# Optimization experiments

Measured on AMD Instinct MI355X. Metric: run time of the kernel, lower is better.

The kernel has to match this reference:

```python
import jax, jax.numpy as jnp
import numpy as np

B, D, H, E, K = 16384, 4096, 2048, 64, 2
TEMPERATURE = 0.8  # training=True


def setup_inputs() -> dict:
    key = jax.random.key(0)
    k1, k2, k3 = jax.random.split(key, 3)
    x = jax.random.normal(k1, (B, D), dtype=jnp.float32)
    W1 = jax.random.normal(k2, (H, D), dtype=jnp.float32) * 0.02
    b1 = jnp.zeros((H,), dtype=jnp.float32)
    W2 = jax.random.normal(k3, (E, H), dtype=jnp.float32) * 0.02
    b2 = jnp.zeros((E,), dtype=jnp.float32)
    return {"x": x, "W1": W1, "b1": b1, "W2": W2, "b2": b2}


def reference(x, W1, b1, W2, b2):
    # router MLP: Linear(D->H) -> ReLU -> Linear(H->E)
    h = jax.nn.relu(jnp.einsum('bd,hd->bh', x, W1) + b1)
    router_logits = jnp.einsum('bh,eh->be', h, W2) + b2  # [B, E]

    # temperature-scaled softmax for routing
    routing_probs = jax.nn.softmax(router_logits / TEMPERATURE, axis=1)
    routing_weights, expert_indices = jax.lax.top_k(routing_probs, K)  # [B, K]
    routing_weights = routing_weights / routing_weights.sum(axis=1, keepdims=True)

    # entropy-based uncertainty uses UN-scaled logits
    full_probs = jax.nn.softmax(router_logits, axis=1)
    entropy = -jnp.sum(full_probs * jnp.log(full_probs + 1e-10), axis=1).mean()
    uncertainty = entropy / jnp.log(jnp.float32(E))
    return routing_weights, expert_indices, uncertainty
```

## Files before the change

kernel.cpp:

```cpp
#include <hip/hip_runtime.h>
#include <hip/hip_bf16.h>
#include <math.h>

#define B_ROWS 16384
#define D_DIM  4096
#define H_DIM  2048
#define E_DIM  64
#define TEMP   0.8f

typedef __bf16 bf16x8 __attribute__((ext_vector_type(8)));
typedef float  f32x4  __attribute__((ext_vector_type(4)));
typedef unsigned short ushort8 __attribute__((ext_vector_type(8)));

__device__ __forceinline__ unsigned short bf_rne(float f) {
  unsigned u = __float_as_uint(f);
  u += 0x7FFF + ((u >> 16) & 1);
  return (unsigned short)(u >> 16);
}

__device__ __forceinline__ void async_copy16(const void* g, void* l) {
  __builtin_amdgcn_global_load_lds(
      (const __attribute__((address_space(1))) void*)g,
      (__attribute__((address_space(3))) void*)l, 16, 0, 0);
}

__global__ __launch_bounds__(256) void split_kernel(
    const float* __restrict__ in, unsigned short* __restrict__ hi,
    unsigned short* __restrict__ lo) {
  const size_t i = ((size_t)blockIdx.x * 256 + threadIdx.x) * 8;
  float4 v0 = *(const float4*)(in + i);
  float4 v1 = *(const float4*)(in + i + 4);
  float f[8] = {v0.x, v0.y, v0.z, v0.w, v1.x, v1.y, v1.z, v1.w};
  ushort8 hv, lv;
#pragma unroll
  for (int j = 0; j < 8; ++j) {
    unsigned short h = bf_rne(f[j]);
    float fh = __uint_as_float(((unsigned)h) << 16);
    hv[j] = h;
    lv[j] = bf_rne(f[j] - fh);
  }
  *(ushort8*)(hi + i) = hv;
  *(ushort8*)(lo + i) = lv;
}

#define G_BM 256
#define G_BN 256
#define G_BK 32
#define G_NT (D_DIM / G_BK)

#define MFMA_TRIPLE(MIv, NIv, FAH, FAL, FBH, FBL)                               \
  _Pragma("unroll")                                                             \
  for (int mf = 0; mf < 4; ++mf) {                                              \
    _Pragma("unroll")                                                           \
    for (int nf = 0; nf < 2; ++nf) {                                            \
      f32x4 a = acc[MIv][mf][NIv][nf];                                          \
      a = __builtin_amdgcn_mfma_f32_16x16x32_bf16(FAH[mf], FBH[nf], a, 0, 0, 0);\
      a = __builtin_amdgcn_mfma_f32_16x16x32_bf16(FAL[mf], FBH[nf], a, 0, 0, 0);\
      a = __builtin_amdgcn_mfma_f32_16x16x32_bf16(FAH[mf], FBL[nf], a, 0, 0, 0);\
      acc[MIv][mf][NIv][nf] = a;                                                \
    }                                                                           \
  }

__global__ __launch_bounds__(512, 2) void gemm1_8ph_kernel(
    const unsigned short* __restrict__ xh, const unsigned short* __restrict__ xl,
    const unsigned short* __restrict__ w1h, const unsigned short* __restrict__ w1l,
    const float* __restrict__ b1,
    unsigned short* __restrict__ hhp, unsigned short* __restrict__ hlp) {
  __shared__ unsigned short LAh[2 * 8192];
  __shared__ unsigned short LAl[2 * 8192];
  __shared__ unsigned short LBh[2 * 8192];
  __shared__ unsigned short LBl[2 * 8192];

  const int t    = threadIdx.x;
  const int lane = t & 63;
  const int w    = t >> 6;
  const int wm   = w >> 2;
  const int wn   = w & 3;

  const int wg   = blockIdx.x;
  const int xcd  = wg & 7;
  const int slot = wg >> 3;
  const int mt   = xcd * 8 + (slot >> 3);
  const int nt   = slot & 7;
  const int m0   = mt * G_BM;
  const int n0   = nt * G_BN;

  const int sr  = t >> 2;
  const int sc  = (t & 3) * 8;
  const int scs = sc ^ (((sr >> 1) & 3) << 3);
  const int t8  = t * 8;
  const unsigned short* gAh = xh  + (size_t)(m0 + sr) * D_DIM + scs;
  const unsigned short* gAl = xl  + (size_t)(m0 + sr) * D_DIM + scs;
  const unsigned short* gBh = w1h + (size_t)(n0 + sr) * D_DIM + scs;
  const unsigned short* gBl = w1l + (size_t)(n0 + sr) * D_DIM + scs;

  auto stageA = [&](int buf, int half, int kt) {
    const size_t go = (size_t)half * 128 * D_DIM + (size_t)kt * G_BK;
    const int lo = buf * 8192 + half * 4096 + t8;
    async_copy16(gAh + go, &LAh[lo]);
    async_copy16(gAl + go, &LAl[lo]);
  };
  auto stageB = [&](int buf, int half, int kt) {
    const size_t go = (size_t)half * 128 * D_DIM + (size_t)kt * G_BK;
    const int lo = buf * 8192 + half * 4096 + t8;
    async_copy16(gBh + go, &LBh[lo]);
    async_copy16(gBl + go, &LBl[lo]);
  };

  constexpr int SST[8] = {0,1,0,1,0,1,0,1};
  constexpr int SHF[8] = {1,1,0,0,1,1,0,0};
  constexpr int SBF[8] = {1,1,0,0,0,0,1,1};
  constexpr int STL[8] = {1,1,2,2,2,2,3,3};

  auto stagePhase = [&](int p, int i) {
    int tl = 2 * i + STL[p];
    if (tl > G_NT - 1) tl = G_NT - 1;
    if (SST[p] == 0) stageA(SBF[p], SHF[p], tl);
    else             stageB(SBF[p], SHF[p], tl);
  };

  const int fr = lane & 15;
  const int ko = (lane >> 4) * 8;
  const int fc = ko ^ (((fr >> 1) & 3) << 3);
  const int aO = (wm * 64 + fr) * 32 + fc;
  const int bO = (wn * 32 + fr) * 32 + fc;

  f32x4 acc[2][4][2][2];
#pragma unroll
  for (int a = 0; a < 2; ++a)
#pragma unroll
    for (int b = 0; b < 4; ++b)
#pragma unroll
      for (int c = 0; c < 2; ++c)
#pragma unroll
        for (int d = 0; d < 2; ++d) acc[a][b][c][d] = (f32x4)0.f;

  stageA(0, 0, 0); stageB(0, 0, 0);
  stageA(0, 1, 0); stageB(0, 1, 0);
  stageA(1, 0, 1); stageB(1, 0, 1);
  asm volatile("s_waitcnt vmcnt(4)" ::: "memory");
  __builtin_amdgcn_s_barrier();
  __builtin_amdgcn_sched_barrier(0);

  for (int i = 0; i < G_NT / 2; ++i) {
#pragma unroll
    for (int half = 0; half < 2; ++half) {
      const int base = half * 4;
      const int cb   = half * 8192;

      bf16x8 fah[4], fal[4];
      bf16x8 fbh0[2], fbl0[2];
      bf16x8 fbh1[2], fbl1[2];

#pragma unroll
      for (int mf = 0; mf < 4; ++mf) {
        fah[mf] = *(const bf16x8*)&LAh[cb + aO + mf * 512];
        fal[mf] = *(const bf16x8*)&LAl[cb + aO + mf * 512];
      }
#pragma unroll
      for (int nf = 0; nf < 2; ++nf) {
        fbh0[nf] = *(const bf16x8*)&LBh[cb + bO + nf * 512];
        fbl0[nf] = *(const bf16x8*)&LBl[cb + bO + nf * 512];
      }
      stagePhase(base + 0, i);
      __builtin_amdgcn_s_barrier();
      __builtin_amdgcn_sched_barrier(0);
      __builtin_amdgcn_s_setprio(1);
      MFMA_TRIPLE(0, 0, fah, fal, fbh0, fbl0)
      __builtin_amdgcn_s_setprio(0);
      __builtin_amdgcn_s_barrier();
      __builtin_amdgcn_sched_barrier(0);

#pragma unroll
      for (int nf = 0; nf < 2; ++nf) {
        fbh1[nf] = *(const bf16x8*)&LBh[cb + 4096 + bO + nf * 512];
        fbl1[nf] = *(const bf16x8*)&LBl[cb + 4096 + bO + nf * 512];
      }
      stagePhase(base + 1, i);
      __builtin_amdgcn_s_barrier();
      __builtin_amdgcn_sched_barrier(0);
      __builtin_amdgcn_s_setprio(1);
      MFMA_TRIPLE(0, 1, fah, fal, fbh1, fbl1)
      __builtin_amdgcn_s_setprio(0);
      __builtin_amdgcn_s_barrier();
      __builtin_amdgcn_sched_barrier(0);

#pragma unroll
      for (int mf = 0; mf < 4; ++mf) {
        fah[mf] = *(const bf16x8*)&LAh[cb + 4096 + aO + mf * 512];
        fal[mf] = *(const bf16x8*)&LAl[cb + 4096 + aO + mf * 512];
      }
      stagePhase(base + 2, i);
      __builtin_amdgcn_s_barrier();
      __builtin_amdgcn_sched_barrier(0);
      __builtin_amdgcn_s_setprio(1);
      MFMA_TRIPLE(1, 0, fah, fal, fbh0, fbl0)
      __builtin_amdgcn_s_setprio(0);
      __builtin_amdgcn_s_barrier();
      __builtin_amdgcn_sched_barrier(0);

      stagePhase(base + 3, i);
      __builtin_amdgcn_s_barrier();
      __builtin_amdgcn_sched_barrier(0);
      __builtin_amdgcn_s_setprio(1);
      MFMA_TRIPLE(1, 1, fah, fal, fbh1, fbl1)
      __builtin_amdgcn_s_setprio(0);
      asm volatile("s_waitcnt vmcnt(4)" ::: "memory");
      __builtin_amdgcn_s_barrier();
      __builtin_amdgcn_sched_barrier(0);
    }
  }
  asm volatile("s_waitcnt vmcnt(0)" ::: "memory");

#pragma unroll
  for (int mi = 0; mi < 2; ++mi)
#pragma unroll
    for (int ni = 0; ni < 2; ++ni)
#pragma unroll
      for (int nf = 0; nf < 2; ++nf) {
        const int nn = n0 + wn * 32 + ni * 128 + nf * 16 + fr;
        const float bias = b1[nn];
#pragma unroll
        for (int mf = 0; mf < 4; ++mf) {
          const int mb = m0 + wm * 64 + mi * 128 + mf * 16 + (lane >> 4) * 4;
#pragma unroll
          for (int r = 0; r < 4; ++r) {
            const float vv = fmaxf(acc[mi][mf][ni][nf][r] + bias, 0.f);
            const unsigned short hv = bf_rne(vv);
            const float fh = __uint_as_float(((unsigned)hv) << 16);
            const unsigned short lv = bf_rne(vv - fh);
            hhp[(size_t)(mb + r) * H_DIM + nn] = hv;
            hlp[(size_t)(mb + r) * H_DIM + nn] = lv;
          }
        }
      }
}

#define BM 128
#define BN 128
#define BKK 32

__global__ __launch_bounds__(256) void gemm1_fb_kernel(
    const float* __restrict__ x,
    const unsigned short* __restrict__ w1h,
    const unsigned short* __restrict__ w1l,
    const float* __restrict__ b1,
    unsigned short* __restrict__ hhp, unsigned short* __restrict__ hlp) {
  __shared__ unsigned short Ah[BM * BKK];
  __shared__ unsigned short Al[BM * BKK];
  __shared__ unsigned short Bh[BN * BKK];
  __shared__ unsigned short Bl[BN * BKK];

  const int t    = threadIdx.x;
  const int lane = t & 63;
  const int w    = t >> 6;
  const int wm   = w >> 1;
  const int wn   = w & 1;
  const int m0   = blockIdx.y * BM;
  const int n0   = blockIdx.x * BN;

  const int e0 = (w * 2 + 0) * 512 + lane * 8;
  const int e1 = (w * 2 + 1) * 512 + lane * 8;
  const int r0 = e0 >> 5, c0 = e0 & 31;
  const int r1 = e1 >> 5, c1 = e1 & 31;
  const unsigned short* bh_g0 = w1h + (size_t)(n0 + r0) * D_DIM + c0;
  const unsigned short* bh_g1 = w1h + (size_t)(n0 + r1) * D_DIM + c1;
  const unsigned short* bl_g0 = w1l + (size_t)(n0 + r0) * D_DIM + c0;
  const unsigned short* bl_g1 = w1l + (size_t)(n0 + r1) * D_DIM + c1;
  unsigned short* bh_l0 = &Bh[e0];
  unsigned short* bh_l1 = &Bh[e1];
  unsigned short* bl_l0 = &Bl[e0];
  unsigned short* bl_l1 = &Bl[e1];

  const int ar = t >> 1;
  const int ac = (t & 1) * 16;
  const float* xp = x + (size_t)(m0 + ar) * D_DIM + ac;
  unsigned short* ah_w = &Ah[ar * BKK + ac];
  unsigned short* al_w = &Al[ar * BKK + ac];

  const int koff = (lane >> 4) * 8;
  const unsigned short* a_rd[4];
  const unsigned short* b_rd[4];
#pragma unroll
  for (int f = 0; f < 4; ++f) {
    a_rd[f] = &Ah[(wm * 64 + f * 16 + (lane & 15)) * BKK + koff];
    b_rd[f] = &Bh[(wn * 64 + f * 16 + (lane & 15)) * BKK + koff];
  }
  const int lo_off_a = (int)(Al - Ah);
  const int lo_off_b = (int)(Bl - Bh);

  f32x4 acc[4][4];
#pragma unroll
  for (int i = 0; i < 4; ++i)
#pragma unroll
    for (int j = 0; j < 4; ++j) acc[i][j] = (f32x4)0.f;

  for (int k0 = 0; k0 < D_DIM; k0 += BKK) {
    async_copy16(bh_g0 + k0, bh_l0);
    async_copy16(bh_g1 + k0, bh_l1);
    async_copy16(bl_g0 + k0, bl_l0);
    async_copy16(bl_g1 + k0, bl_l1);

    float4 v[4];
#pragma unroll
    for (int j = 0; j < 4; ++j) v[j] = *(const float4*)(xp + k0 + j * 4);
    float f[16] = {v[0].x, v[0].y, v[0].z, v[0].w, v[1].x, v[1].y, v[1].z, v[1].w,
                   v[2].x, v[2].y, v[2].z, v[2].w, v[3].x, v[3].y, v[3].z, v[3].w};
    ushort8 hv0, hv1, lv0, lv1;
#pragma unroll
    for (int j = 0; j < 8; ++j) {
      unsigned short h = bf_rne(f[j]);
      float fh = __uint_as_float(((unsigned)h) << 16);
      hv0[j] = h;
      lv0[j] = bf_rne(f[j] - fh);
    }
#pragma unroll
    for (int j = 0; j < 8; ++j) {
      unsigned short h = bf_rne(f[8 + j]);
      float fh = __uint_as_float(((unsigned)h) << 16);
      hv1[j] = h;
      lv1[j] = bf_rne(f[8 + j] - fh);
    }
    *(ushort8*)(ah_w)     = hv0;
    *(ushort8*)(ah_w + 8) = hv1;
    *(ushort8*)(al_w)     = lv0;
    *(ushort8*)(al_w + 8) = lv1;

    __syncthreads();

    bf16x8 fa_h[4], fa_l[4], fb_h[4], fb_l[4];
#pragma unroll
    for (int ff = 0; ff < 4; ++ff) {
      fa_h[ff] = *(const bf16x8*)(a_rd[ff]);
      fa_l[ff] = *(const bf16x8*)(a_rd[ff] + lo_off_a);
      fb_h[ff] = *(const bf16x8*)(b_rd[ff]);
      fb_l[ff] = *(const bf16x8*)(b_rd[ff] + lo_off_b);
    }
#pragma unroll
    for (int i = 0; i < 4; ++i)
#pragma unroll
      for (int j = 0; j < 4; ++j) {
        acc[i][j] = __builtin_amdgcn_mfma_f32_16x16x32_bf16(fa_h[i], fb_h[j], acc[i][j], 0, 0, 0);
        acc[i][j] = __builtin_amdgcn_mfma_f32_16x16x32_bf16(fa_l[i], fb_h[j], acc[i][j], 0, 0, 0);
        acc[i][j] = __builtin_amdgcn_mfma_f32_16x16x32_bf16(fa_h[i], fb_l[j], acc[i][j], 0, 0, 0);
      }
    __syncthreads();
  }

#pragma unroll
  for (int fn = 0; fn < 4; ++fn) {
    const int n = n0 + wn * 64 + fn * 16 + (lane & 15);
    const float bias = b1[n];
#pragma unroll
    for (int fm = 0; fm < 4; ++fm) {
      const int mbase = m0 + wm * 64 + fm * 16 + (lane >> 4) * 4;
#pragma unroll
      for (int r = 0; r < 4; ++r) {
        const float vv = fmaxf(acc[fm][fn][r] + bias, 0.f);
        const unsigned short hv = bf_rne(vv);
        const float fh = __uint_as_float(((unsigned)hv) << 16);
        const unsigned short lv = bf_rne(vv - fh);
        hhp[(size_t)(mbase + r) * H_DIM + n] = hv;
        hlp[(size_t)(mbase + r) * H_DIM + n] = lv;
      }
    }
  }
}

#define F_BM 64
#define F_BK 64
#define F_NT (H_DIM / F_BK)

__global__ __launch_bounds__(256) void gemm2_router_kernel(
    const unsigned short* __restrict__ hhp,
    const unsigned short* __restrict__ hlp,
    const unsigned short* __restrict__ w2h,
    const unsigned short* __restrict__ w2l,
    const float* __restrict__ b2,
    float* __restrict__ out, float* __restrict__ accum) {
  __shared__ unsigned short Ahs[2 * 4096];
  __shared__ unsigned short Als[2 * 4096];
  __shared__ unsigned short Bhs[2 * 4096];
  __shared__ unsigned short Bls[2 * 4096];
  __shared__ float LG[F_BM][E_DIM + 1];

  const int t    = threadIdx.x;
  const int lane = t & 63;
  const int w    = t >> 6;
  const int m0   = blockIdx.x * F_BM;

  const int srow = w * 8 + (lane >> 3);
  const int scol = ((lane & 7) * 8) ^ (((lane >> 3) & 7) << 3);
  const int t8   = t * 8;
  const unsigned short* gAh = hhp + (size_t)(m0 + srow) * H_DIM + scol;
  const unsigned short* gAl = hlp + (size_t)(m0 + srow) * H_DIM + scol;
  const unsigned short* gBh = w2h + (size_t)srow * H_DIM + scol;
  const unsigned short* gBl = w2l + (size_t)srow * H_DIM + scol;

  auto stage2 = [&](int buf, int kt) {
    const size_t k0 = (size_t)kt * F_BK;
#pragma unroll
    for (int c = 0; c < 2; ++c) {
      const size_t go = k0 + (size_t)c * 32 * H_DIM;
      const int lo = buf * 4096 + c * 2048 + t8;
      async_copy16(gAh + go, &Ahs[lo]);
      async_copy16(gAl + go, &Als[lo]);
      async_copy16(gBh + go, &Bhs[lo]);
      async_copy16(gBl + go, &Bls[lo]);
    }
  };

  const int fr = lane & 15;
  const int ko = (lane >> 4) * 8;
  const int Ra = w * 16 + fr;
  int aoff[2], boff[2][4];
#pragma unroll
  for (int kk = 0; kk < 2; ++kk) {
    aoff[kk] = Ra * 64 + ((kk * 32 + ko) ^ ((Ra & 7) << 3));
#pragma unroll
    for (int f = 0; f < 4; ++f) {
      const int Rb = f * 16 + fr;
      boff[kk][f] = Rb * 64 + ((kk * 32 + ko) ^ ((Rb & 7) << 3));
    }
  }

  f32x4 acc[4];
#pragma unroll
  for (int f = 0; f < 4; ++f) acc[f] = (f32x4)0.f;

  stage2(0, 0);
  int buf = 0;
  for (int kt = 0; kt < F_NT; ++kt) {
    if (kt + 1 < F_NT) {
      stage2(buf ^ 1, kt + 1);
      asm volatile("s_waitcnt vmcnt(8)" ::: "memory");
    } else {
      asm volatile("s_waitcnt vmcnt(0)" ::: "memory");
    }
    __builtin_amdgcn_s_barrier();
    __builtin_amdgcn_sched_barrier(0);
    const int bo = buf * 4096;
#pragma unroll
    for (int kk = 0; kk < 2; ++kk) {
      bf16x8 fa_h = *(const bf16x8*)&Ahs[bo + aoff[kk]];
      bf16x8 fa_l = *(const bf16x8*)&Als[bo + aoff[kk]];
#pragma unroll
      for (int f = 0; f < 4; ++f) {
        bf16x8 fb_h = *(const bf16x8*)&Bhs[bo + boff[kk][f]];
        bf16x8 fb_l = *(const bf16x8*)&Bls[bo + boff[kk][f]];
        acc[f] = __builtin_amdgcn_mfma_f32_16x16x32_bf16(fa_h, fb_h, acc[f], 0, 0, 0);
        acc[f] = __builtin_amdgcn_mfma_f32_16x16x32_bf16(fa_l, fb_h, acc[f], 0, 0, 0);
        acc[f] = __builtin_amdgcn_mfma_f32_16x16x32_bf16(fa_h, fb_l, acc[f], 0, 0, 0);
      }
    }
    __builtin_amdgcn_s_barrier();
    __builtin_amdgcn_sched_barrier(0);
    buf ^= 1;
  }

#pragma unroll
  for (int f = 0; f < 4; ++f) {
    const int e = f * 16 + fr;
    const float bias = b2[e];
#pragma unroll
    for (int r = 0; r < 4; ++r) {
      const int ml = w * 16 + (lane >> 4) * 4 + r;
      LG[ml][e] = acc[f][r] + bias;
    }
  }
  __syncthreads();

  if (t < F_BM) {
    const int row = m0 + t;
    float l0 = LG[t][0]; int i0 = 0;
    float l1 = -INFINITY; int i1 = -1;
#pragma unroll
    for (int e = 1; e < E_DIM; ++e) {
      float v = LG[t][e];
      if (v > l0)      { l1 = l0; i1 = i0; l0 = v; i0 = e; }
      else if (v > l1) { l1 = v; i1 = e; }
    }

    const float eT = expf((l1 - l0) / TEMP);
    const float w0 = 1.f / (1.f + eT);
    const float w1 = eT / (1.f + eT);

    float Z = 0.f;
#pragma unroll
    for (int e = 0; e < E_DIM; ++e) Z += expf(LG[t][e] - l0);
    const float invZ = 1.f / Z;
    float ent = 0.f;
#pragma unroll
    for (int e = 0; e < E_DIM; ++e) {
      float p = expf(LG[t][e] - l0) * invZ;
      ent -= p * logf(p + 1e-10f);
    }

    out[(size_t)row * 2 + 0] = w0;
    out[(size_t)row * 2 + 1] = w1;
    out[(size_t)B_ROWS * 2 + (size_t)row * 2 + 0] = (float)i0;
    out[(size_t)B_ROWS * 2 + (size_t)row * 2 + 1] = (float)i1;

#pragma unroll
    for (int off = 32; off > 0; off >>= 1) ent += __shfl_down(ent, off);
    if (t == 0) atomicAdd(accum, ent);
  }
}

__global__ void zero_kernel(float* p) { p[0] = 0.f; }

__global__ void finalize_kernel(const float* __restrict__ accum,
                                float* __restrict__ out) {
  out[(size_t)B_ROWS * 4] = accum[0] / ((float)B_ROWS * logf((float)E_DIM));
}

extern "C" void kernel_launch(void* const* d_in, const int* in_sizes, int n_in,
                              void* d_out, int out_size, void* d_ws,
                              size_t ws_size, hipStream_t stream) {
  const float* x  = (const float*)d_in[0];
  const float* W1 = (const float*)d_in[1];
  const float* b1 = (const float*)d_in[2];
  const float* W2 = (const float*)d_in[3];
  const float* b2 = (const float*)d_in[4];
  float* out = (float*)d_out;

  const size_t SZ_W1 = (size_t)H_DIM * D_DIM;
  const size_t SZ_W2 = (size_t)E_DIM * H_DIM;
  const size_t SZ_H  = (size_t)B_ROWS * H_DIM;
  const size_t SZ_X  = (size_t)B_ROWS * D_DIM;

  unsigned short* w1h = (unsigned short*)d_ws;
  unsigned short* w1l = w1h + SZ_W1;
  unsigned short* w2h = w1l + SZ_W1;
  unsigned short* w2l = w2h + SZ_W2;
  unsigned short* hhp = w2l + SZ_W2;
  unsigned short* hlp = hhp + SZ_H;
  float* accum        = (float*)(hlp + SZ_H);
  unsigned short* xh  = (unsigned short*)(accum + 64);
  unsigned short* xl  = xh + SZ_X;
  const size_t need_bytes = (size_t)((char*)(xl + SZ_X) - (char*)d_ws);
  const bool fast = ws_size >= need_bytes;

  zero_kernel<<<1, 1, 0, stream>>>(accum);

  split_kernel<<<(int)(SZ_W1 / (256 * 8)), 256, 0, stream>>>(W1, w1h, w1l);
  split_kernel<<<(int)(SZ_W2 / (256 * 8)), 256, 0, stream>>>(W2, w2h, w2l);

  if (fast) {
    split_kernel<<<(int)(SZ_X / (256 * 8)), 256, 0, stream>>>(x, xh, xl);
    gemm1_8ph_kernel<<<512, 512, 0, stream>>>(xh, xl, w1h, w1l, b1, hhp, hlp);
  } else {
    dim3 g1f(H_DIM / BN, B_ROWS / BM);
    gemm1_fb_kernel<<<g1f, 256, 0, stream>>>(x, w1h, w1l, b1, hhp, hlp);
  }

  gemm2_router_kernel<<<B_ROWS / F_BM, 256, 0, stream>>>(hhp, hlp, w2h, w2l, b2,
                                                         out, accum);

  finalize_kernel<<<1, 1, 0, stream>>>(accum, out);
}
```

Before: 1.076 ms.

## Software-pipeline LDS fragment loads ahead of MFMA phases with double register sets

Splits the A fragments into two register sets and issues LDS reads for the next phase's fragments before the current phase's MFMAs, including prefetching the next half-buffer's A/B fragments during the last phase. This hides LDS read latency behind matrix ops instead of serializing reads and MFMA between barriers. It raises VGPR pressure, which could lower occupancy or cause spills, and moves the vmcnt wait earlier.

```diff
diff --git a/kernel.cpp b/kernel.cpp
--- a/kernel.cpp
+++ b/kernel.cpp
@@ -142,70 +142,81 @@
   __builtin_amdgcn_s_barrier();
   __builtin_amdgcn_sched_barrier(0);
 
+  bf16x8 fah0[4], fal0[4], fah1[4], fal1[4];
+  bf16x8 fbh0[2], fbl0[2], fbh1[2], fbl1[2];
+
+#pragma unroll
+  for (int mf = 0; mf < 4; ++mf) {
+    fah0[mf] = *(const bf16x8*)&LAh[aO + mf * 512];
+    fal0[mf] = *(const bf16x8*)&LAl[aO + mf * 512];
+  }
+#pragma unroll
+  for (int nf = 0; nf < 2; ++nf) {
+    fbh0[nf] = *(const bf16x8*)&LBh[bO + nf * 512];
+    fbl0[nf] = *(const bf16x8*)&LBl[bO + nf * 512];
+  }
+
   for (int i = 0; i < G_NT / 2; ++i) {
 #pragma unroll
     for (int half = 0; half < 2; ++half) {
       const int base = half * 4;
       const int cb   = half * 8192;
-
-      bf16x8 fah[4], fal[4];
-      bf16x8 fbh0[2], fbl0[2];
-      bf16x8 fbh1[2], fbl1[2];
-
-#pragma unroll
-      for (int mf = 0; mf < 4; ++mf) {
-        fah[mf] = *(const bf16x8*)&LAh[cb + aO + mf * 512];
-        fal[mf] = *(const bf16x8*)&LAl[cb + aO + mf * 512];
-      }
-#pragma unroll
-      for (int nf = 0; nf < 2; ++nf) {
-        fbh0[nf] = *(const bf16x8*)&LBh[cb + bO + nf * 512];
-        fbl0[nf] = *(const bf16x8*)&LBl[cb + bO + nf * 512];
-      }
+      const int cbn  = cb ^ 8192;
+
       stagePhase(base + 0, i);
       __builtin_amdgcn_s_barrier();
       __builtin_amdgcn_sched_barrier(0);
-      __builtin_amdgcn_s_setprio(1);
-      MFMA_TRIPLE(0, 0, fah, fal, fbh0, fbl0)
-      __builtin_amdgcn_s_setprio(0);
-      __builtin_amdgcn_s_barrier();
-      __builtin_amdgcn_sched_barrier(0);
-
 #pragma unroll
       for (int nf = 0; nf < 2; ++nf) {
         fbh1[nf] = *(const bf16x8*)&LBh[cb + 4096 + bO + nf * 512];
         fbl1[nf] = *(const bf16x8*)&LBl[cb + 4096 + bO + nf * 512];
       }
+      __builtin_amdgcn_s_setprio(1);
+      MFMA_TRIPLE(0, 0, fah0, fal0, fbh0, fbl0)
+      __builtin_amdgcn_s_setprio(0);
+      __builtin_amdgcn_s_barrier();
+      __builtin_amdgcn_sched_barrier(0);
+
       stagePhase(base + 1, i);
       __builtin_amdgcn_s_barrier();
       __builtin_amdgcn_sched_barrier(0);
+#pragma unroll
+      for (int mf = 0; mf < 4; ++mf) {
+        fah1[mf] = *(const bf16x8*)&LAh[cb + 4096 + aO + mf * 512];
+        fal1[mf] = *(const bf16x8*)&LAl[cb + 4096 + aO + mf * 512];
+      }
       __builtin_amdgcn_s_setprio(1);
-      MFMA_TRIPLE(0, 1, fah, fal, fbh1, fbl1)
+      MFMA_TRIPLE(0, 1, fah0, fal0, fbh1, fbl1)
       __builtin_amdgcn_s_setprio(0);
       __builtin_amdgcn_s_barrier();
       __builtin_amdgcn_sched_barrier(0);
 
+      stagePhase(base + 2, i);
+      __builtin_amdgcn_s_barrier();
+      __builtin_amdgcn_sched_barrier(0);
+      __builtin_amdgcn_s_setprio(1);
+      MFMA_TRIPLE(1, 0, fah1, fal1, fbh0, fbl0)
+      __builtin_amdgcn_s_setprio(0);
+      __builtin_amdgcn_s_barrier();
+      __builtin_amdgcn_sched_barrier(0);
+
+      stagePhase(base + 3, i);
+      __builtin_amdgcn_s_barrier();
+      __builtin_amdgcn_sched_barrier(0);
+      asm volatile("s_waitcnt vmcnt(4)" ::: "memory");
 #pragma unroll
       for (int mf = 0; mf < 4; ++mf) {
-        fah[mf] = *(const bf16x8*)&LAh[cb + 4096 + aO + mf * 512];
-        fal[mf] = *(const bf16x8*)&LAl[cb + 4096 + aO + mf * 512];
-      }
-      stagePhase(base + 2, i);
-      __builtin_amdgcn_s_barrier();
-      __builtin_amdgcn_sched_barrier(0);
+        fah0[mf] = *(const bf16x8*)&LAh[cbn + aO + mf * 512];
+        fal0[mf] = *(const bf16x8*)&LAl[cbn + aO + mf * 512];
+      }
+#pragma unroll
+      for (int nf = 0; nf < 2; ++nf) {
+        fbh0[nf] = *(const bf16x8*)&LBh[cbn + bO + nf * 512];
+        fbl0[nf] = *(const bf16x8*)&LBl[cbn + bO + nf * 512];
+      }
       __builtin_amdgcn_s_setprio(1);
-      MFMA_TRIPLE(1, 0, fah, fal, fbh0, fbl0)
+      MFMA_TRIPLE(1, 1, fah1, fal1, fbh1, fbl1)
       __builtin_amdgcn_s_setprio(0);
-      __builtin_amdgcn_s_barrier();
-      __builtin_amdgcn_sched_barrier(0);
-
-      stagePhase(base + 3, i);
-      __builtin_amdgcn_s_barrier();
-      __builtin_amdgcn_sched_barrier(0);
-      __builtin_amdgcn_s_setprio(1);
-      MFMA_TRIPLE(1, 1, fah, fal, fbh1, fbl1)
-      __builtin_amdgcn_s_setprio(0);
-      asm volatile("s_waitcnt vmcnt(4)" ::: "memory");
       __builtin_amdgcn_s_barrier();
       __builtin_amdgcn_sched_barrier(0);
     }
```

After: 1.169 ms. 1.09x slower.

## Fuse second router GEMM into first GEMM epilogue with per-tile partial logits

Applied to the files above, without the earlier changes.

The first GEMM's epilogue no longer writes the hidden activation (hi/lo bf16 split) to global memory. It stages each 256x256 h tile in swizzled LDS and immediately multiplies it by the matching W2 slice with MFMA, writing partial logits per N-tile. A new lightweight router kernel sums the 8 partials, adds the bias, and computes the top-2, softmax and entropy. This removes the large h write and re-read in exchange for extra LDS traffic, synchronisation in the epilogue, and W2 reads issued straight from global memory.

```diff
diff --git a/kernel.cpp b/kernel.cpp
--- a/kernel.cpp
+++ b/kernel.cpp
@@ -65,11 +65,13 @@
     const unsigned short* __restrict__ xh, const unsigned short* __restrict__ xl,
     const unsigned short* __restrict__ w1h, const unsigned short* __restrict__ w1l,
     const float* __restrict__ b1,
-    unsigned short* __restrict__ hhp, unsigned short* __restrict__ hlp) {
-  __shared__ unsigned short LAh[2 * 8192];
-  __shared__ unsigned short LAl[2 * 8192];
-  __shared__ unsigned short LBh[2 * 8192];
-  __shared__ unsigned short LBl[2 * 8192];
+    const unsigned short* __restrict__ w2h, const unsigned short* __restrict__ w2l,
+    float* __restrict__ logitsP) {
+  __shared__ unsigned short SMEM[65536];
+  unsigned short* const LAh = SMEM;
+  unsigned short* const LAl = SMEM + 16384;
+  unsigned short* const LBh = SMEM + 32768;
+  unsigned short* const LBl = SMEM + 49152;
 
   const int t    = threadIdx.x;
   const int lane = t & 63;
@@ -211,29 +213,131 @@
     }
   }
   asm volatile("s_waitcnt vmcnt(0)" ::: "memory");
-
-#pragma unroll
-  for (int mi = 0; mi < 2; ++mi)
+  __syncthreads();
+
+  unsigned short* const Hh = SMEM;
+  unsigned short* const Hl = SMEM + 32768;
+
+#pragma unroll
+  for (int mi = 0; mi < 2; ++mi) {
 #pragma unroll
     for (int ni = 0; ni < 2; ++ni)
 #pragma unroll
       for (int nf = 0; nf < 2; ++nf) {
-        const int nn = n0 + wn * 32 + ni * 128 + nf * 16 + fr;
-        const float bias = b1[nn];
+        const int colb = wn * 32 + ni * 128 + nf * 16 + fr;
+        const float bias = b1[n0 + colb];
+        const int u = colb >> 3, j = colb & 7;
 #pragma unroll
         for (int mf = 0; mf < 4; ++mf) {
-          const int mb = m0 + wm * 64 + mi * 128 + mf * 16 + (lane >> 4) * 4;
+          const int rowb = wm * 64 + mf * 16 + (lane >> 4) * 4;
 #pragma unroll
           for (int r = 0; r < 4; ++r) {
+            const int rr = rowb + r;
             const float vv = fmaxf(acc[mi][mf][ni][nf][r] + bias, 0.f);
             const unsigned short hv = bf_rne(vv);
             const float fh = __uint_as_float(((unsigned)hv) << 16);
             const unsigned short lv = bf_rne(vv - fh);
-            hhp[(size_t)(mb + r) * H_DIM + nn] = hv;
-            hlp[(size_t)(mb + r) * H_DIM + nn] = lv;
+            const int a = rr * 256 + ((u ^ (rr & 7)) << 3) + j;
+            Hh[a] = hv;
+            Hl[a] = lv;
           }
         }
       }
+    __syncthreads();
+
+    f32x4 lac[4];
+#pragma unroll
+    for (int nf = 0; nf < 4; ++nf) lac[nf] = (f32x4)0.f;
+
+    const int arow = w * 16 + fr;
+#pragma unroll
+    for (int kf = 0; kf < 8; ++kf) {
+      const int au = (kf * 4 + (lane >> 4)) ^ (arow & 7);
+      bf16x8 ahi = *(const bf16x8*)&Hh[arow * 256 + au * 8];
+      bf16x8 alo = *(const bf16x8*)&Hl[arow * 256 + au * 8];
+#pragma unroll
+      for (int nf = 0; nf < 4; ++nf) {
+        const size_t boff = (size_t)(nf * 16 + fr) * H_DIM + n0 + kf * 32 + ko;
+        bf16x8 bhi = *(const bf16x8*)(w2h + boff);
+        bf16x8 blo = *(const bf16x8*)(w2l + boff);
+        lac[nf] = __builtin_amdgcn_mfma_f32_16x16x32_bf16(ahi, bhi, lac[nf], 0, 0, 0);
+        lac[nf] = __builtin_amdgcn_mfma_f32_16x16x32_bf16(alo, bhi, lac[nf], 0, 0, 0);
+        lac[nf] = __builtin_amdgcn_mfma_f32_16x16x32_bf16(ahi, blo, lac[nf], 0, 0, 0);
+      }
+    }
+
+    float* lpb = logitsP + (size_t)nt * ((size_t)B_ROWS * E_DIM);
+#pragma unroll
+    for (int nf = 0; nf < 4; ++nf) {
+      const int e = nf * 16 + fr;
+#pragma unroll
+      for (int r = 0; r < 4; ++r) {
+        const int grow = m0 + mi * 128 + w * 16 + (lane >> 4) * 4 + r;
+        lpb[(size_t)grow * E_DIM + e] = lac[nf][r];
+      }
+    }
+    __syncthreads();
+  }
+}
+
+__global__ __launch_bounds__(256) void router_kernel(
+    const float* __restrict__ lp, const float* __restrict__ b2,
+    float* __restrict__ out, float* __restrict__ accum) {
+  const int t = threadIdx.x;
+  const size_t row = (size_t)blockIdx.x * 256 + t;
+  const size_t PS = (size_t)B_ROWS * E_DIM;
+
+  float lg[64];
+#pragma unroll
+  for (int e4 = 0; e4 < 16; ++e4) {
+    float4 v = *(const float4*)(lp + row * E_DIM + e4 * 4);
+    lg[e4 * 4 + 0] = v.x; lg[e4 * 4 + 1] = v.y;
+    lg[e4 * 4 + 2] = v.z; lg[e4 * 4 + 3] = v.w;
+  }
+#pragma unroll
+  for (int p = 1; p < 8; ++p) {
+#pragma unroll
+    for (int e4 = 0; e4 < 16; ++e4) {
+      float4 v = *(const float4*)(lp + (size_t)p * PS + row * E_DIM + e4 * 4);
+      lg[e4 * 4 + 0] += v.x; lg[e4 * 4 + 1] += v.y;
+      lg[e4 * 4 + 2] += v.z; lg[e4 * 4 + 3] += v.w;
+    }
+  }
+#pragma unroll
+  for (int e = 0; e < E_DIM; ++e) lg[e] += b2[e];
+
+  float l0 = lg[0]; int i0 = 0;
+  float l1 = -INFINITY; int i1 = -1;
+#pragma unroll
+  for (int e = 1; e < E_DIM; ++e) {
+    float v = lg[e];
+    if (v > l0)      { l1 = l0; i1 = i0; l0 = v; i0 = e; }
+    else if (v > l1) { l1 = v; i1 = e; }
+  }
+
+  const float eT = expf((l1 - l0) / TEMP);
+  const float w0 = 1.f / (1.f + eT);
+  const float w1 = eT / (1.f + eT);
+
+  float Z = 0.f;
+#pragma unroll
+  for (int e = 0; e < E_DIM; ++e) Z += expf(lg[e] - l0);
+  const float invZ = 1.f / Z;
+  float ent = 0.f;
+#pragma unroll
+  for (int e = 0; e < E_DIM; ++e) {
+    float p = expf(lg[e] - l0) * invZ;
+    ent -= p * logf(p + 1e-10f);
+  }
+
+  out[row * 2 + 0] = w0;
+  out[row * 2 + 1] = w1;
+  out[(size_t)B_ROWS * 2 + row * 2 + 0] = (float)i0;
+  out[(size_t)B_ROWS * 2 + row * 2 + 1] = (float)i1;
+
+#pragma unroll
+  for (int off = 32; off > 0; off >>= 1) ent += __shfl_down(ent, off);
+  if ((t & 63) == 0) atomicAdd(accum, ent);
 }
 
 #define BM 128
@@ -535,6 +639,7 @@
   unsigned short* w2l = w2h + SZ_W2;
   unsigned short* hhp = w2l + SZ_W2;
   unsigned short* hlp = hhp + SZ_H;
+  float* logitsP      = (float*)hhp;
   float* accum        = (float*)(hlp + SZ_H);
   unsigned short* xh  = (unsigned short*)(accum + 64);
   unsigned short* xl  = xh + SZ_X;
@@ -548,14 +653,15 @@
 
   if (fast) {
     split_kernel<<<(int)(SZ_X / (256 * 8)), 256, 0, stream>>>(x, xh, xl);
-    gemm1_8ph_kernel<<<512, 512, 0, stream>>>(xh, xl, w1h, w1l, b1, hhp, hlp);
+    gemm1_8ph_kernel<<<512, 512, 0, stream>>>(xh, xl, w1h, w1l, b1,
+                                              w2h, w2l, logitsP);
+    router_kernel<<<B_ROWS / 256, 256, 0, stream>>>(logitsP, b2, out, accum);
   } else {
     dim3 g1f(H_DIM / BN, B_ROWS / BM);
     gemm1_fb_kernel<<<g1f, 256, 0, stream>>>(x, w1h, w1l, b1, hhp, hlp);
-  }
-
-  gemm2_router_kernel<<<B_ROWS / F_BM, 256, 0, stream>>>(hhp, hlp, w2h, w2l, b2,
-                                                         out, accum);
+    gemm2_router_kernel<<<B_ROWS / F_BM, 256, 0, stream>>>(hhp, hlp, w2h, w2l,
+                                                           b2, out, accum);
+  }
 
   finalize_kernel<<<1, 1, 0, stream>>>(accum, out);
 }
```

After: 1.043 ms. 1.03x faster.
